# Performance work log

Measured on AMD Instinct MI355X. Metric: run time of the kernel, lower is better.

## Reference

```python
import jax, jax.numpy as jnp
import numpy as np

SPIKE_THRESHOLD = 0.01


def setup_inputs() -> dict:
    key = jax.random.key(0)
    k_x, k_w1, k_w2 = jax.random.split(key, 3)
    B, T, S, D, F = 4, 16, 512, 512, 2048
    x = jax.random.normal(k_x, (B, T, S, D), dtype=jnp.float32)
    # FFN parameters (the wrapped `model`): Linear(D,F) -> ReLU -> Linear(F,D)
    w1 = jax.random.normal(k_w1, (D, F), dtype=jnp.float32) * (1.0 / np.sqrt(D))
    b1 = jnp.zeros((F,), dtype=jnp.float32)
    w2 = jax.random.normal(k_w2, (F, D), dtype=jnp.float32) * (1.0 / np.sqrt(F))
    b2 = jnp.zeros((D,), dtype=jnp.float32)
    return {"x": x, "w1": w1, "b1": b1, "w2": w2, "b2": b2}


def reference(x, w1, b1, w2, b2):
    # x: [B, T, S, D]. Event-driven: rows with any |x| > threshold are
    # processed by the model; inactive rows produce zeros.
    spike_mask = jnp.any(jnp.abs(x) > SPIKE_THRESHOLD, axis=-1)  # [B, T, S]
    h = jax.nn.relu(jnp.einsum("btsd,df->btsf", x, w1) + b1)     # [B, T, S, F]
    y = jnp.einsum("btsf,fd->btsd", h, w2) + b2                   # [B, T, S, D]
    return jnp.where(spike_mask[..., None], y, jnp.zeros((), dtype=y.dtype))
```

## Files before the change

### kernel.cpp

```cpp
#include <hip/hip_runtime.h>
#include <hip/hip_bf16.h>

typedef __attribute__((ext_vector_type(8))) short bf16x8;
typedef __attribute__((ext_vector_type(4))) float f32x4;

#define TH 0.01f
#define MFMA(a, b, c) __builtin_amdgcn_mfma_f32_16x16x32_bf16(a, b, c, 0, 0, 0)

constexpr int D  = 512;
constexpr int F  = 2048;
constexpr int NC = 32;

static __device__ __forceinline__ short f2bf(float f) {
  union { float f; unsigned u; } v; v.f = f;
  unsigned r = v.u + 0x7FFFu + ((v.u >> 16) & 1u);
  return (short)(r >> 16);
}

static __device__ __forceinline__ void gl16(const void* g, char* l) {
  __builtin_amdgcn_global_load_lds(
      (const __attribute__((address_space(1))) unsigned*)g,
      (__attribute__((address_space(3))) unsigned*)l, 16, 0, 0);
}

__global__ void prep_weights(const float* __restrict__ w1, const float* __restrict__ w2,
                             short* __restrict__ w1s, short* __restrict__ w2s) {
  int g = blockIdx.x * 256 + threadIdx.x;
  if (g < 131072) {
    int region = g >> 11, chunk = region >> 1, half = region & 1;
    int q0  = (g & 2047) << 3;
    int col = q0 >> 8;
    int kb  = ((q0 & 255) ^ ((col & 7) << 3)) + (half << 8);
    int fcol = (chunk << 6) + col;
    bf16x8 v;
#pragma unroll
    for (int j = 0; j < 8; ++j) v[j] = f2bf(w1[(size_t)(kb + j) * F + fcol]);
    *(bf16x8*)(w1s + (size_t)g * 8) = v;
  } else {
    int h = g - 131072;
    int region = h >> 11, chunk = region >> 1, sub = region & 1;
    int q0  = (h & 2047) << 3;
    int col = q0 >> 5;
    int kb  = ((q0 & 31) ^ (((col >> 1) & 3) << 3)) + (chunk << 6) + (sub << 5);
    bf16x8 v;
#pragma unroll
    for (int j = 0; j < 8; ++j) v[j] = f2bf(w2[(size_t)(kb + j) * D + col]);
    *(bf16x8*)(w2s + (size_t)h * 8) = v;
  }
}

__global__ __launch_bounds__(512, 2)
void ffn_fused(const float* __restrict__ x,
               const float* __restrict__ b1,
               const float* __restrict__ b2,
               const char* __restrict__ w1g,
               const char* __restrict__ w2g,
               float* __restrict__ out) {
  extern __shared__ char smem[];
  short*    w1s0 = (short*)(smem);
  short*    w1s1 = (short*)(smem + 32768);
  short*    w2p0 = (short*)(smem + 65536);
  short*    w2p1 = (short*)(smem + 98304);
  short*    hs   = (short*)(smem + 131072);
  float*    b1s  = (float*)(smem + 140288);
  float*    b2s  = (float*)(smem + 148480);
  unsigned* spk  = (unsigned*)(smem + 150528);

  const int tid  = threadIdx.x;
  const int lane = tid & 63, wid = tid >> 6;
  const int l15  = lane & 15, lk = lane >> 4;
  const int row0 = blockIdx.x * 64;

#pragma unroll
  for (int t = 0; t < 8; ++t)
    gl16(w1g + (size_t)(t * 512 + tid) * 16, smem + (t * 512 + tid) * 16);

  *(float4*)&b1s[tid * 4] = *(const float4*)&b1[tid * 4];
  if (tid < 128) *(float4*)&b2s[tid * 4] = *(const float4*)&b2[tid * 4];

  const int xrow = (wid & 3) * 16 + l15;
  const float* xp = x + (size_t)(row0 + xrow) * D + lk * 8;
  bf16x8 xr[16];
  bool any = false;
#pragma unroll
  for (int ks = 0; ks < 16; ++ks) {
    float4 f0 = *(const float4*)(xp + ks * 32);
    float4 f1 = *(const float4*)(xp + ks * 32 + 4);
    any = any | (fabsf(f0.x) > TH) | (fabsf(f0.y) > TH) | (fabsf(f0.z) > TH) |
          (fabsf(f0.w) > TH) | (fabsf(f1.x) > TH) | (fabsf(f1.y) > TH) |
          (fabsf(f1.z) > TH) | (fabsf(f1.w) > TH);
    bf16x8 v;
    v[0] = f2bf(f0.x); v[1] = f2bf(f0.y); v[2] = f2bf(f0.z); v[3] = f2bf(f0.w);
    v[4] = f2bf(f1.x); v[5] = f2bf(f1.y); v[6] = f2bf(f1.z); v[7] = f2bf(f1.w);
    xr[ks] = v;
  }
  unsigned a = any ? 1u : 0u;
  a |= __shfl_xor(a, 16, 64);
  a |= __shfl_xor(a, 32, 64);
  if (wid < 4 && lane < 16) spk[xrow] = a;

  asm volatile("s_waitcnt vmcnt(4) lgkmcnt(0)" ::: "memory");
  __builtin_amdgcn_s_barrier();

  const int c00 = (wid >> 2) * 32;
  const int c01 = c00 + 16;
  const int R0  = (wid >> 2) * 32;
  const int C0  = (wid & 3) * 128;

  f32x4 oacc[2][8];
#pragma unroll
  for (int m = 0; m < 2; ++m)
#pragma unroll
    for (int n = 0; n < 8; ++n) oacc[m][n] = f32x4{0.f, 0.f, 0.f, 0.f};

  for (int i = 0; i < NC; ++i) {
    f32x4 h0 = {0.f, 0.f, 0.f, 0.f}, h1 = {0.f, 0.f, 0.f, 0.f};

    {
      const char* src = w2g + (size_t)i * 65536;
#pragma unroll
      for (int t = 0; t < 8; ++t)
        gl16(src + (size_t)(t * 512 + tid) * 16, smem + 65536 + (t * 512 + tid) * 16);
    }
    __builtin_amdgcn_s_setprio(1);
#pragma unroll
    for (int s = 0; s < 8; ++s) {
      int o0 = ((c00 + l15) << 8) + (s << 5) + (lk << 3); o0 ^= ((c00 + l15) & 7) << 3;
      int o1 = ((c01 + l15) << 8) + (s << 5) + (lk << 3); o1 ^= ((c01 + l15) & 7) << 3;
      h0 = MFMA(*(const bf16x8*)(w1s0 + o0), xr[s], h0);
      h1 = MFMA(*(const bf16x8*)(w1s0 + o1), xr[s], h1);
    }
    __builtin_amdgcn_s_setprio(0);
    asm volatile("s_waitcnt vmcnt(8) lgkmcnt(0)" ::: "memory");
    __builtin_amdgcn_s_barrier();

    if (i + 1 < NC) {
      const char* src = w1g + (size_t)(i + 1) * 65536;
#pragma unroll
      for (int t = 0; t < 4; ++t)
        gl16(src + (size_t)(t * 512 + tid) * 16, smem + (t * 512 + tid) * 16);
    }
    __builtin_amdgcn_s_setprio(1);
#pragma unroll
    for (int s = 0; s < 8; ++s) {
      int o0 = ((c00 + l15) << 8) + (s << 5) + (lk << 3); o0 ^= ((c00 + l15) & 7) << 3;
      int o1 = ((c01 + l15) << 8) + (s << 5) + (lk << 3); o1 ^= ((c01 + l15) & 7) << 3;
      h0 = MFMA(*(const bf16x8*)(w1s1 + o0), xr[s + 8], h0);
      h1 = MFMA(*(const bf16x8*)(w1s1 + o1), xr[s + 8], h1);
    }
    __builtin_amdgcn_s_setprio(0);
    {
      float4 bv0 = *(const float4*)&b1s[i * 64 + c00 + lk * 4];
      float4 bv1 = *(const float4*)&b1s[i * 64 + c01 + lk * 4];
      short4 p0, p1;
      p0.x = f2bf(fmaxf(h0[0] + bv0.x, 0.f)); p0.y = f2bf(fmaxf(h0[1] + bv0.y, 0.f));
      p0.z = f2bf(fmaxf(h0[2] + bv0.z, 0.f)); p0.w = f2bf(fmaxf(h0[3] + bv0.w, 0.f));
      p1.x = f2bf(fmaxf(h1[0] + bv1.x, 0.f)); p1.y = f2bf(fmaxf(h1[1] + bv1.y, 0.f));
      p1.z = f2bf(fmaxf(h1[2] + bv1.z, 0.f)); p1.w = f2bf(fmaxf(h1[3] + bv1.w, 0.f));
      *(short4*)&hs[xrow * 72 + c00 + lk * 4] = p0;
      *(short4*)&hs[xrow * 72 + c01 + lk * 4] = p1;
    }
    if (i + 1 < NC) asm volatile("s_waitcnt vmcnt(4) lgkmcnt(0)" ::: "memory");
    else            asm volatile("s_waitcnt vmcnt(0) lgkmcnt(0)" ::: "memory");
    __builtin_amdgcn_s_barrier();

    if (i + 1 < NC) {
      const char* src = w1g + (size_t)(i + 1) * 65536 + 32768;
#pragma unroll
      for (int t = 0; t < 4; ++t)
        gl16(src + (size_t)(t * 512 + tid) * 16, smem + 32768 + (t * 512 + tid) * 16);
    }
    __builtin_amdgcn_s_setprio(1);
#pragma unroll
    for (int ks = 0; ks < 2; ++ks) {
      const short* w2p = ks ? w2p1 : w2p0;
      bf16x8 a0 = *(const bf16x8*)&hs[(R0 + l15) * 72 + ks * 32 + lk * 8];
      bf16x8 a1 = *(const bf16x8*)&hs[(R0 + 16 + l15) * 72 + ks * 32 + lk * 8];
#pragma unroll
      for (int fn = 0; fn < 8; ++fn) {
        int col = C0 + fn * 16 + l15;
        int o = (col << 5) + (lk << 3); o ^= ((col >> 1) & 3) << 3;
        bf16x8 g = *(const bf16x8*)(w2p + o);
        oacc[0][fn] = MFMA(a0, g, oacc[0][fn]);
        oacc[1][fn] = MFMA(a1, g, oacc[1][fn]);
      }
    }
    __builtin_amdgcn_s_setprio(0);
    if (i + 1 < NC) {
      asm volatile("s_waitcnt vmcnt(4) lgkmcnt(0)" ::: "memory");
      __builtin_amdgcn_s_barrier();
    }
  }

  unsigned s0[4], s1[4];
#pragma unroll
  for (int r = 0; r < 4; ++r) {
    s0[r] = spk[R0 + lk * 4 + r];
    s1[r] = spk[R0 + 16 + lk * 4 + r];
  }
#pragma unroll
  for (int fn = 0; fn < 8; ++fn) {
    int col = C0 + fn * 16 + l15;
    float bias = b2s[col];
#pragma unroll
    for (int r = 0; r < 4; ++r) {
      int row = R0 + lk * 4 + r;
      float v = oacc[0][fn][r] + bias;
      out[(size_t)(row0 + row) * D + col] = s0[r] ? v : 0.f;
    }
#pragma unroll
    for (int r = 0; r < 4; ++r) {
      int row = R0 + 16 + lk * 4 + r;
      float v = oacc[1][fn][r] + bias;
      out[(size_t)(row0 + row) * D + col] = s1[r] ? v : 0.f;
    }
  }
}

extern "C" void kernel_launch(void* const* d_in, const int* in_sizes, int n_in,
                              void* d_out, int out_size, void* d_ws, size_t ws_size,
                              hipStream_t stream) {
  const float* x  = (const float*)d_in[0];
  const float* w1 = (const float*)d_in[1];
  const float* b1 = (const float*)d_in[2];
  const float* w2 = (const float*)d_in[3];
  const float* b2 = (const float*)d_in[4];
  float* out = (float*)d_out;

  short* w1staged = (short*)d_ws;
  short* w2staged = w1staged + (size_t)D * F;

  prep_weights<<<1024, 256, 0, stream>>>(w1, w2, w1staged, w2staged);

  static_assert(sizeof(float4) == 16, "");
  (void)hipFuncSetAttribute((const void*)ffn_fused,
                            hipFuncAttributeMaxDynamicSharedMemorySize, 150784);
  int M = out_size / D;
  ffn_fused<<<M / 64, 512, 150784, stream>>>(x, b1, b2, (const char*)w1staged,
                                             (const char*)w2staged, out);
}
```

Baseline: 186.1 us.

## Double row tile to 128 per block with per-wave full-width output ownership

Each block now handles 128 rows instead of 64, and each of the 8 waves owns 16 rows across all 512 output columns. Every wave computes all 64 hidden columns of a chunk for its own rows. Streamed W1/W2 chunks are reused across twice as many rows, which halves weight traffic from L2/HBM per output row. The weight loads become a four-slot rolling pipeline of 32KB quarter-chunks with a barrier per quarter. The cost is more accumulator registers (32 output tiles per wave), which may hurt occupancy at launch bounds 512x2, and half as many blocks (512) to spread over the CUs.

```diff
diff --git a/kernel.cpp b/kernel.cpp
--- a/kernel.cpp
+++ b/kernel.cpp
@@ -7,9 +7,17 @@
 #define TH 0.01f
 #define MFMA(a, b, c) __builtin_amdgcn_mfma_f32_16x16x32_bf16(a, b, c, 0, 0, 0)
 
-constexpr int D  = 512;
-constexpr int F  = 2048;
-constexpr int NC = 32;
+constexpr int D = 512, F = 2048, BM = 128, NC = 32;
+
+constexpr int W1A_O = 0;
+constexpr int W1B_O = 32768;
+constexpr int W2A_O = 65536;
+constexpr int W2B_O = 98304;
+constexpr int HS_O  = 131072;
+constexpr int B1_O  = 147456;
+constexpr int B2_O  = 155648;
+constexpr int SPK_O = 157696;
+constexpr int LDS_TOTAL = 158208;
 
 static __device__ __forceinline__ short f2bf(float f) {
   union { float f; unsigned u; } v; v.f = f;
@@ -25,29 +33,62 @@
 
 __global__ void prep_weights(const float* __restrict__ w1, const float* __restrict__ w2,
                              short* __restrict__ w1s, short* __restrict__ w2s) {
-  int g = blockIdx.x * 256 + threadIdx.x;
-  if (g < 131072) {
-    int region = g >> 11, chunk = region >> 1, half = region & 1;
-    int q0  = (g & 2047) << 3;
-    int col = q0 >> 8;
-    int kb  = ((q0 & 255) ^ ((col & 7) << 3)) + (half << 8);
-    int fcol = (chunk << 6) + col;
+  int G = blockIdx.x * 256 + threadIdx.x;
+  if (G < 131072) {
+    int region = G >> 11, g = G & 2047;
+    int chunk = region >> 1, half = region & 1;
+    int col = g >> 5, s = g & 31;
+    int kbase = half * 256 + (s ^ (col & 7)) * 8;
+    int fcol = chunk * 64 + col;
     bf16x8 v;
 #pragma unroll
-    for (int j = 0; j < 8; ++j) v[j] = f2bf(w1[(size_t)(kb + j) * F + fcol]);
-    *(bf16x8*)(w1s + (size_t)g * 8) = v;
+    for (int j = 0; j < 8; ++j) v[j] = f2bf(w1[(size_t)(kbase + j) * F + fcol]);
+    *(bf16x8*)(w1s + (size_t)G * 8) = v;
   } else {
-    int h = g - 131072;
-    int region = h >> 11, chunk = region >> 1, sub = region & 1;
-    int q0  = (h & 2047) << 3;
-    int col = q0 >> 5;
-    int kb  = ((q0 & 31) ^ (((col >> 1) & 3) << 3)) + (chunk << 6) + (sub << 5);
+    int H = G - 131072;
+    int region = H >> 11, g = H & 2047;
+    int chunk = region >> 1, sub = region & 1;
+    int col = g >> 2, kg = g & 3;
+    int fbase = chunk * 64 + sub * 32 + (kg ^ ((col >> 1) & 3)) * 8;
     bf16x8 v;
 #pragma unroll
-    for (int j = 0; j < 8; ++j) v[j] = f2bf(w2[(size_t)(kb + j) * D + col]);
-    *(bf16x8*)(w2s + (size_t)h * 8) = v;
-  }
-}
+    for (int j = 0; j < 8; ++j) v[j] = f2bf(w2[(size_t)(fbase + j) * D + col]);
+    *(bf16x8*)(w2s + (size_t)H * 8) = v;
+  }
+}
+
+#define ISSUE4(loff, gptr)                                                      \
+  do {                                                                          \
+    _Pragma("unroll") for (int _t = 0; _t < 4; ++_t)                            \
+        gl16((const char*)(gptr) + (size_t)(_t * 512 + tid) * 16,               \
+             smem + (loff) + (_t * 512 + tid) * 16);                            \
+  } while (0)
+
+#define G1_HALF(SLOT, KB)                                                       \
+  do {                                                                          \
+    const short* _ws = (const short*)(smem + (SLOT));                           \
+    __builtin_amdgcn_s_setprio(1);                                              \
+    _Pragma("unroll") for (int s = 0; s < 8; ++s) {                             \
+      _Pragma("unroll") for (int f = 0; f < 4; ++f) {                           \
+        int _hcol = f * 16 + l15;                                               \
+        int _off = _hcol * 256 + (((s * 4 + lk) ^ (_hcol & 7)) << 3);           \
+        hacc[f] = MFMA(*(const bf16x8*)(_ws + _off), xr[(KB) + s], hacc[f]);    \
+      }                                                                         \
+    }                                                                           \
+    __builtin_amdgcn_s_setprio(0);                                              \
+  } while (0)
+
+#define G2_SUB(W2OFF, SUB)                                                      \
+  do {                                                                          \
+    const short* _h = (const short*)(smem + HS_O);                              \
+    const short* _w = (const short*)(smem + (W2OFF));                           \
+    bf16x8 _af = *(const bf16x8*)(_h + hrow * 64 +                              \
+                                  ((((SUB)*4 + lk) ^ (hrow & 7)) << 3));        \
+    __builtin_amdgcn_s_setprio(1);                                              \
+    _Pragma("unroll") for (int fn = 0; fn < 32; ++fn)                           \
+      oacc[fn] = MFMA(_af, *(const bf16x8*)(_w + fn * 512 + w2base), oacc[fn]); \
+    __builtin_amdgcn_s_setprio(0);                                              \
+  } while (0)
 
 __global__ __launch_bounds__(512, 2)
 void ffn_fused(const float* __restrict__ x,
@@ -57,162 +98,105 @@
                const char* __restrict__ w2g,
                float* __restrict__ out) {
   extern __shared__ char smem[];
-  short*    w1s0 = (short*)(smem);
-  short*    w1s1 = (short*)(smem + 32768);
-  short*    w2p0 = (short*)(smem + 65536);
-  short*    w2p1 = (short*)(smem + 98304);
-  short*    hs   = (short*)(smem + 131072);
-  float*    b1s  = (float*)(smem + 140288);
-  float*    b2s  = (float*)(smem + 148480);
-  unsigned* spk  = (unsigned*)(smem + 150528);
-
-  const int tid  = threadIdx.x;
+  float*    b1s = (float*)(smem + B1_O);
+  float*    b2s = (float*)(smem + B2_O);
+  unsigned* spk = (unsigned*)(smem + SPK_O);
+
+  const int tid = threadIdx.x;
   const int lane = tid & 63, wid = tid >> 6;
-  const int l15  = lane & 15, lk = lane >> 4;
-  const int row0 = blockIdx.x * 64;
-
-#pragma unroll
-  for (int t = 0; t < 8; ++t)
-    gl16(w1g + (size_t)(t * 512 + tid) * 16, smem + (t * 512 + tid) * 16);
+  const int l15 = lane & 15, lk = lane >> 4;
+  const int row0 = blockIdx.x * BM;
+
+  ISSUE4(W1A_O, w1g);
+  ISSUE4(W1B_O, w1g + 32768);
+  ISSUE4(W2A_O, w2g);
 
   *(float4*)&b1s[tid * 4] = *(const float4*)&b1[tid * 4];
   if (tid < 128) *(float4*)&b2s[tid * 4] = *(const float4*)&b2[tid * 4];
 
-  const int xrow = (wid & 3) * 16 + l15;
-  const float* xp = x + (size_t)(row0 + xrow) * D + lk * 8;
   bf16x8 xr[16];
-  bool any = false;
-#pragma unroll
-  for (int ks = 0; ks < 16; ++ks) {
-    float4 f0 = *(const float4*)(xp + ks * 32);
-    float4 f1 = *(const float4*)(xp + ks * 32 + 4);
-    any = any | (fabsf(f0.x) > TH) | (fabsf(f0.y) > TH) | (fabsf(f0.z) > TH) |
-          (fabsf(f0.w) > TH) | (fabsf(f1.x) > TH) | (fabsf(f1.y) > TH) |
-          (fabsf(f1.z) > TH) | (fabsf(f1.w) > TH);
-    bf16x8 v;
-    v[0] = f2bf(f0.x); v[1] = f2bf(f0.y); v[2] = f2bf(f0.z); v[3] = f2bf(f0.w);
-    v[4] = f2bf(f1.x); v[5] = f2bf(f1.y); v[6] = f2bf(f1.z); v[7] = f2bf(f1.w);
-    xr[ks] = v;
-  }
-  unsigned a = any ? 1u : 0u;
-  a |= __shfl_xor(a, 16, 64);
-  a |= __shfl_xor(a, 32, 64);
-  if (wid < 4 && lane < 16) spk[xrow] = a;
-
-  asm volatile("s_waitcnt vmcnt(4) lgkmcnt(0)" ::: "memory");
-  __builtin_amdgcn_s_barrier();
-
-  const int c00 = (wid >> 2) * 32;
-  const int c01 = c00 + 16;
-  const int R0  = (wid >> 2) * 32;
-  const int C0  = (wid & 3) * 128;
-
-  f32x4 oacc[2][8];
-#pragma unroll
-  for (int m = 0; m < 2; ++m)
-#pragma unroll
-    for (int n = 0; n < 8; ++n) oacc[m][n] = f32x4{0.f, 0.f, 0.f, 0.f};
+  {
+    const float* xp = x + (size_t)(row0 + wid * 16 + l15) * D + lk * 8;
+    bool any = false;
+#pragma unroll
+    for (int s = 0; s < 16; ++s) {
+      float4 f0 = *(const float4*)(xp + s * 32);
+      float4 f1 = *(const float4*)(xp + s * 32 + 4);
+      any = any | (fabsf(f0.x) > TH) | (fabsf(f0.y) > TH) | (fabsf(f0.z) > TH) |
+            (fabsf(f0.w) > TH) | (fabsf(f1.x) > TH) | (fabsf(f1.y) > TH) |
+            (fabsf(f1.z) > TH) | (fabsf(f1.w) > TH);
+      bf16x8 v;
+      v[0] = f2bf(f0.x); v[1] = f2bf(f0.y); v[2] = f2bf(f0.z); v[3] = f2bf(f0.w);
+      v[4] = f2bf(f1.x); v[5] = f2bf(f1.y); v[6] = f2bf(f1.z); v[7] = f2bf(f1.w);
+      xr[s] = v;
+    }
+    unsigned a = any ? 1u : 0u;
+    a |= __shfl_xor(a, 16, 64);
+    a |= __shfl_xor(a, 32, 64);
+    if (lane < 16) spk[wid * 16 + lane] = a;
+  }
+
+  f32x4 oacc[32];
+#pragma unroll
+  for (int n = 0; n < 32; ++n) oacc[n] = f32x4{0.f, 0.f, 0.f, 0.f};
+
+  const int w2base = l15 * 32 + ((lk ^ ((l15 >> 1) & 3)) << 3);
+  const int hrow = wid * 16 + l15;
+  const int hxor = (hrow & 7) << 3;
 
   for (int i = 0; i < NC; ++i) {
-    f32x4 h0 = {0.f, 0.f, 0.f, 0.f}, h1 = {0.f, 0.f, 0.f, 0.f};
-
+    f32x4 hacc[4];
+
+    asm volatile("s_waitcnt vmcnt(8) lgkmcnt(0)" ::: "memory");
+    __builtin_amdgcn_s_barrier();
+    ISSUE4(W2B_O, w2g + (size_t)(i * 2 + 1) * 32768);
+#pragma unroll
+    for (int f = 0; f < 4; ++f) hacc[f] = f32x4{0.f, 0.f, 0.f, 0.f};
+    G1_HALF(W1A_O, 0);
+
+    asm volatile("s_waitcnt vmcnt(8) lgkmcnt(0)" ::: "memory");
+    __builtin_amdgcn_s_barrier();
+    if (i < NC - 1) ISSUE4(W1A_O, w1g + (size_t)((i + 1) * 2) * 32768);
+    G1_HALF(W1B_O, 8);
     {
-      const char* src = w2g + (size_t)i * 65536;
-#pragma unroll
-      for (int t = 0; t < 8; ++t)
-        gl16(src + (size_t)(t * 512 + tid) * 16, smem + 65536 + (t * 512 + tid) * 16);
-    }
-    __builtin_amdgcn_s_setprio(1);
-#pragma unroll
-    for (int s = 0; s < 8; ++s) {
-      int o0 = ((c00 + l15) << 8) + (s << 5) + (lk << 3); o0 ^= ((c00 + l15) & 7) << 3;
-      int o1 = ((c01 + l15) << 8) + (s << 5) + (lk << 3); o1 ^= ((c01 + l15) & 7) << 3;
-      h0 = MFMA(*(const bf16x8*)(w1s0 + o0), xr[s], h0);
-      h1 = MFMA(*(const bf16x8*)(w1s0 + o1), xr[s], h1);
-    }
-    __builtin_amdgcn_s_setprio(0);
-    asm volatile("s_waitcnt vmcnt(8) lgkmcnt(0)" ::: "memory");
-    __builtin_amdgcn_s_barrier();
-
-    if (i + 1 < NC) {
-      const char* src = w1g + (size_t)(i + 1) * 65536;
-#pragma unroll
-      for (int t = 0; t < 4; ++t)
-        gl16(src + (size_t)(t * 512 + tid) * 16, smem + (t * 512 + tid) * 16);
-    }
-    __builtin_amdgcn_s_setprio(1);
-#pragma unroll
-    for (int s = 0; s < 8; ++s) {
-      int o0 = ((c00 + l15) << 8) + (s << 5) + (lk << 3); o0 ^= ((c00 + l15) & 7) << 3;
-      int o1 = ((c01 + l15) << 8) + (s << 5) + (lk << 3); o1 ^= ((c01 + l15) & 7) << 3;
-      h0 = MFMA(*(const bf16x8*)(w1s1 + o0), xr[s + 8], h0);
-      h1 = MFMA(*(const bf16x8*)(w1s1 + o1), xr[s + 8], h1);
-    }
-    __builtin_amdgcn_s_setprio(0);
-    {
-      float4 bv0 = *(const float4*)&b1s[i * 64 + c00 + lk * 4];
-      float4 bv1 = *(const float4*)&b1s[i * 64 + c01 + lk * 4];
-      short4 p0, p1;
-      p0.x = f2bf(fmaxf(h0[0] + bv0.x, 0.f)); p0.y = f2bf(fmaxf(h0[1] + bv0.y, 0.f));
-      p0.z = f2bf(fmaxf(h0[2] + bv0.z, 0.f)); p0.w = f2bf(fmaxf(h0[3] + bv0.w, 0.f));
-      p1.x = f2bf(fmaxf(h1[0] + bv1.x, 0.f)); p1.y = f2bf(fmaxf(h1[1] + bv1.y, 0.f));
-      p1.z = f2bf(fmaxf(h1[2] + bv1.z, 0.f)); p1.w = f2bf(fmaxf(h1[3] + bv1.w, 0.f));
-      *(short4*)&hs[xrow * 72 + c00 + lk * 4] = p0;
-      *(short4*)&hs[xrow * 72 + c01 + lk * 4] = p1;
-    }
-    if (i + 1 < NC) asm volatile("s_waitcnt vmcnt(4) lgkmcnt(0)" ::: "memory");
-    else            asm volatile("s_waitcnt vmcnt(0) lgkmcnt(0)" ::: "memory");
-    __builtin_amdgcn_s_barrier();
-
-    if (i + 1 < NC) {
-      const char* src = w1g + (size_t)(i + 1) * 65536 + 32768;
-#pragma unroll
-      for (int t = 0; t < 4; ++t)
-        gl16(src + (size_t)(t * 512 + tid) * 16, smem + 32768 + (t * 512 + tid) * 16);
-    }
-    __builtin_amdgcn_s_setprio(1);
-#pragma unroll
-    for (int ks = 0; ks < 2; ++ks) {
-      const short* w2p = ks ? w2p1 : w2p0;
-      bf16x8 a0 = *(const bf16x8*)&hs[(R0 + l15) * 72 + ks * 32 + lk * 8];
-      bf16x8 a1 = *(const bf16x8*)&hs[(R0 + 16 + l15) * 72 + ks * 32 + lk * 8];
-#pragma unroll
-      for (int fn = 0; fn < 8; ++fn) {
-        int col = C0 + fn * 16 + l15;
-        int o = (col << 5) + (lk << 3); o ^= ((col >> 1) & 3) << 3;
-        bf16x8 g = *(const bf16x8*)(w2p + o);
-        oacc[0][fn] = MFMA(a0, g, oacc[0][fn]);
-        oacc[1][fn] = MFMA(a1, g, oacc[1][fn]);
+      short* hsl = (short*)(smem + HS_O);
+#pragma unroll
+      for (int f = 0; f < 4; ++f) {
+        float4 bv = *(const float4*)&b1s[i * 64 + f * 16 + lk * 4];
+        short4 p;
+        p.x = f2bf(fmaxf(hacc[f][0] + bv.x, 0.f));
+        p.y = f2bf(fmaxf(hacc[f][1] + bv.y, 0.f));
+        p.z = f2bf(fmaxf(hacc[f][2] + bv.z, 0.f));
+        p.w = f2bf(fmaxf(hacc[f][3] + bv.w, 0.f));
+        *(short4*)&hsl[hrow * 64 + ((f * 16 + lk * 4) ^ hxor)] = p;
       }
     }
-    __builtin_amdgcn_s_setprio(0);
-    if (i + 1 < NC) {
-      asm volatile("s_waitcnt vmcnt(4) lgkmcnt(0)" ::: "memory");
-      __builtin_amdgcn_s_barrier();
-    }
-  }
-
-  unsigned s0[4], s1[4];
-#pragma unroll
-  for (int r = 0; r < 4; ++r) {
-    s0[r] = spk[R0 + lk * 4 + r];
-    s1[r] = spk[R0 + 16 + lk * 4 + r];
-  }
-#pragma unroll
-  for (int fn = 0; fn < 8; ++fn) {
-    int col = C0 + fn * 16 + l15;
+
+    if (i < NC - 1) asm volatile("s_waitcnt vmcnt(8) lgkmcnt(0)" ::: "memory");
+    else            asm volatile("s_waitcnt vmcnt(4) lgkmcnt(0)" ::: "memory");
+    __builtin_amdgcn_s_barrier();
+    if (i < NC - 1) ISSUE4(W1B_O, w1g + (size_t)((i + 1) * 2 + 1) * 32768);
+    G2_SUB(W2A_O, 0);
+
+    if (i < NC - 1) asm volatile("s_waitcnt vmcnt(8) lgkmcnt(0)" ::: "memory");
+    else            asm volatile("s_waitcnt vmcnt(0) lgkmcnt(0)" ::: "memory");
+    __builtin_amdgcn_s_barrier();
+    if (i < NC - 1) ISSUE4(W2A_O, w2g + (size_t)((i + 1) * 2) * 32768);
+    G2_SUB(W2B_O, 1);
+  }
+
+  unsigned sv[4];
+#pragma unroll
+  for (int r = 0; r < 4; ++r) sv[r] = spk[wid * 16 + lk * 4 + r];
+#pragma unroll
+  for (int fn = 0; fn < 32; ++fn) {
+    int col = fn * 16 + l15;
     float bias = b2s[col];
 #pragma unroll
     for (int r = 0; r < 4; ++r) {
-      int row = R0 + lk * 4 + r;
-      float v = oacc[0][fn][r] + bias;
-      out[(size_t)(row0 + row) * D + col] = s0[r] ? v : 0.f;
-    }
-#pragma unroll
-    for (int r = 0; r < 4; ++r) {
-      int row = R0 + 16 + lk * 4 + r;
-      float v = oacc[1][fn][r] + bias;
-      out[(size_t)(row0 + row) * D + col] = s1[r] ? v : 0.f;
+      int row = wid * 16 + lk * 4 + r;
+      float v = oacc[fn][r] + bias;
+      out[(size_t)(row0 + row) * D + col] = sv[r] ? v : 0.f;
     }
   }
 }
@@ -232,10 +216,9 @@
 
   prep_weights<<<1024, 256, 0, stream>>>(w1, w2, w1staged, w2staged);
 
-  static_assert(sizeof(float4) == 16, "");
   (void)hipFuncSetAttribute((const void*)ffn_fused,
-                            hipFuncAttributeMaxDynamicSharedMemorySize, 150784);
+                            hipFuncAttributeMaxDynamicSharedMemorySize, LDS_TOTAL);
   int M = out_size / D;
-  ffn_fused<<<M / 64, 512, 150784, stream>>>(x, b1, b2, (const char*)w1staged,
-                                             (const char*)w2staged, out);
-}
+  ffn_fused<<<M / BM, 512, LDS_TOTAL, stream>>>(x, b1, b2, (const char*)w1staged,
+                                                (const char*)w2staged, out);
+}
```

Result: faster. 165.8 us (-10.9%).
